# Optimization experiments

Hardware: AMD Instinct MI355X
Metric: run time of the kernel (lower is better)

## Reference

```python
import jax, jax.numpy as jnp
import numpy as np

B, C = 20000, 8          # trees, children (leaves) per tree
WORD, TAG, MEM = 300, 50, 150


def gru_cell(x, h, w_ih, w_hh, b_ih, b_hh):
    # torch.nn.GRUCell math; gate order r, z, n
    gi = x @ w_ih.T + b_ih
    gh = h @ w_hh.T + b_hh
    ir, iz, i_n = jnp.split(gi, 3, axis=-1)
    hr, hz, hn = jnp.split(gh, 3, axis=-1)
    r = jax.nn.sigmoid(ir + hr)
    z = jax.nn.sigmoid(iz + hz)
    n = jnp.tanh(i_n + r * hn)
    return (1.0 - z) * n + z * h


def setup_inputs() -> dict:
    key = jax.random.key(0)
    ks = jax.random.split(key, 16)
    s = 0.05  # small init scale for weights
    return {
        "embs": jax.random.normal(ks[0], (B, C, WORD), jnp.float32),
        "tags": jax.random.normal(ks[1], (B, C, TAG), jnp.float32),
        "tag_parent": jax.random.normal(ks[2], (B, TAG), jnp.float32),
        "w_ih_leaf": jax.random.normal(ks[3], (3 * MEM, WORD + TAG), jnp.float32) * s,
        "w_hh_leaf": jax.random.normal(ks[4], (3 * MEM, MEM), jnp.float32) * s,
        "b_ih_leaf": jax.random.normal(ks[5], (3 * MEM,), jnp.float32) * s,
        "b_hh_leaf": jax.random.normal(ks[6], (3 * MEM,), jnp.float32) * s,
        "w_ih_child": jax.random.normal(ks[7], (3 * MEM, MEM + 2 * TAG), jnp.float32) * s,
        "w_hh_child": jax.random.normal(ks[8], (3 * MEM, MEM), jnp.float32) * s,
        "b_ih_child": jax.random.normal(ks[9], (3 * MEM,), jnp.float32) * s,
        "b_hh_child": jax.random.normal(ks[10], (3 * MEM,), jnp.float32) * s,
        "w_ih_node": jax.random.normal(ks[11], (3 * MEM, 1), jnp.float32) * s,
        "w_hh_node": jax.random.normal(ks[12], (3 * MEM, MEM), jnp.float32) * s,
        "b_ih_node": jax.random.normal(ks[13], (3 * MEM,), jnp.float32) * s,
        "b_hh_node": jax.random.normal(ks[14], (3 * MEM,), jnp.float32) * s,
    }


def reference(embs, tags, tag_parent,
              w_ih_leaf, w_hh_leaf, b_ih_leaf, b_hh_leaf,
              w_ih_child, w_hh_child, b_ih_child, b_hh_child,
              w_ih_node, w_hh_node, b_ih_node, b_hh_node):
    # 1) all leaves at once: GRUCell(concat(word, tag), h=0)  -> [B, C, MEM]
    x_leaf = jnp.concatenate([embs, tags], axis=-1)            # [B, C, WORD+TAG]
    h0 = jnp.zeros((B, C, MEM), x_leaf.dtype)
    leaf_h = gru_cell(x_leaf, h0, w_ih_leaf, w_hh_leaf, b_ih_leaf, b_hh_leaf)

    # 2) child inputs: concat(child state, child tag, parent tag)  -> [B, C, MEM+2*TAG]
    tp = jnp.broadcast_to(tag_parent[:, None, :], (B, C, TAG))
    x_child = jnp.concatenate([leaf_h, tags, tp], axis=-1)

    # 3) sequential left-to-right fold over children with children GRUCell
    def step(h, x_i):
        h_new = gru_cell(x_i, h, w_ih_child, w_hh_child, b_ih_child, b_hh_child)
        return h_new, None

    h_init = jnp.zeros((B, MEM), x_leaf.dtype)
    h_final, _ = jax.lax.scan(step, h_init, jnp.swapaxes(x_child, 0, 1))  # scan over C

    # 4) node GRUCell with x = zeros(1)
    x_zeros = jnp.zeros((B, 1), x_leaf.dtype)
    root = gru_cell(x_zeros, h_final, w_ih_node, w_hh_node, b_ih_node, b_hh_node)
    return root  # [B, MEM]
```

## Files before the change

### kernel.cpp

```cpp
#include <hip/hip_runtime.h>


typedef _Float16 f16;
typedef _Float16 f16x4 __attribute__((ext_vector_type(4)));
typedef _Float16 f16x8 __attribute__((ext_vector_type(8)));
typedef float f32x4 __attribute__((ext_vector_type(4)));

namespace {

constexpr int NTREE = 20000;
constexpr int CCH   = 8;
constexpr int WORD  = 300;
constexpr int TAGD  = 50;
constexpr int MEMD  = 150;
constexpr int NBLK  = 250;
constexpr int LBLK  = 625;

constexpr int KT_L = 11;
constexpr int KT_I = 8;
constexpr int KT_H = 5;
constexpr int KT_N = 5;
constexpr int NTILE = 30;

constexpr size_t OFF_WL   = 0;
constexpr size_t OFF_WI   = OFF_WL + (size_t)KT_L * NTILE * 64 * 16;
constexpr size_t OFF_WH   = OFF_WI + (size_t)KT_I * NTILE * 64 * 16;
constexpr size_t OFF_WN   = OFF_WH + (size_t)KT_H * NTILE * 64 * 16;
constexpr size_t OFF_BIAS = OFF_WN + (size_t)KT_N * NTILE * 64 * 16;
constexpr size_t OFF_DATA = OFF_BIAS + 16 * 160 * 4;

constexpr size_t TG_BYTES = 15360;
constexpr size_t C_STRIDE = (size_t)1250 * TG_BYTES;
constexpr size_t GI_BYTES = (size_t)CCH * C_STRIDE;
constexpr size_t WS_R3    = OFF_DATA + GI_BYTES;
constexpr int    HW_S  = 152;
constexpr size_t WS_R2 = OFF_DATA + (size_t)CCH * NTREE * HW_S * 2;


__device__ __forceinline__ float sigmoid_f(float x) {
  return 1.0f / (1.0f + __expf(-x));
}
__device__ __forceinline__ float tanh_f(float x) {
  float ax = fabsf(x);
  float e  = __expf(-2.0f * ax);
  float t  = (1.0f - e) / (1.0f + e);
  return copysignf(t, x);
}

__global__ void prep_kernel(const float* __restrict__ w_ih_leaf,
                            const float* __restrict__ b_ih_leaf,
                            const float* __restrict__ b_hh_leaf,
                            const float* __restrict__ w_ih_child,
                            const float* __restrict__ w_hh_child,
                            const float* __restrict__ b_ih_child,
                            const float* __restrict__ b_hh_child,
                            const float* __restrict__ w_hh_node,
                            const float* __restrict__ b_ih_node,
                            const float* __restrict__ b_hh_node,
                            char* __restrict__ ws) {
  const int NWL = KT_L * NTILE * 64;
  const int NWI = KT_I * NTILE * 64;
  const int NWH = KT_H * NTILE * 64;
  const int NWN = KT_N * NTILE * 64;
  int t = blockIdx.x * blockDim.x + threadIdx.x;

  if (t < NWL) {
    int kt = t / (NTILE * 64), rem = t % (NTILE * 64);
    int nt = rem / 64, l = rem % 64;
    int gate = nt / 10, jt = nt % 10;
    int j = jt * 16 + (l & 15);
    bool valid = j < MEMD;
    int g = gate * MEMD + (valid ? j : 0);
    f16x8 v;
#pragma unroll
    for (int e = 0; e < 8; ++e) {
      int k = kt * 32 + ((l >> 4) * 8) + e;
      v[e] = (f16)((valid && k < WORD + TAGD) ? w_ih_leaf[g * (WORD + TAGD) + k] : 0.0f);
    }
    ((f16x8*)(ws + OFF_WL))[t] = v;
    return;
  }
  t -= NWL;
  if (t < NWI) {
    int kt = t / (NTILE * 64), rem = t % (NTILE * 64);
    int nt = rem / 64, l = rem % 64;
    int gate = nt / 10, jt = nt % 10;
    int j = jt * 16 + (l & 15);
    bool valid = j < MEMD;
    int g = gate * MEMD + (valid ? j : 0);
    f16x8 v;
#pragma unroll
    for (int e = 0; e < 8; ++e) {
      int k = kt * 32 + ((l >> 4) * 8) + e;
      int src = (k < 150) ? k : (k >= 152 && k < 252) ? (k - 2) : -1;
      v[e] = (f16)((valid && src >= 0) ? w_ih_child[g * 250 + src] : 0.0f);
    }
    ((f16x8*)(ws + OFF_WI))[t] = v;
    return;
  }
  t -= NWI;
  if (t < NWH) {
    int kt = t / (NTILE * 64), rem = t % (NTILE * 64);
    int nt = rem / 64, l = rem % 64;
    int gate = nt / 10, jt = nt % 10;
    int j = jt * 16 + (l & 15);
    bool valid = j < MEMD;
    int g = gate * MEMD + (valid ? j : 0);
    f16x8 v;
#pragma unroll
    for (int e = 0; e < 8; ++e) {
      int k = kt * 32 + ((l >> 4) * 8) + e;
      v[e] = (f16)((valid && k < MEMD) ? w_hh_child[g * MEMD + k] : 0.0f);
    }
    ((f16x8*)(ws + OFF_WH))[t] = v;
    return;
  }
  t -= NWH;
  if (t < NWN) {
    int kt = t / (NTILE * 64), rem = t % (NTILE * 64);
    int nt = rem / 64, l = rem % 64;
    int gate = nt / 10, jt = nt % 10;
    int j = jt * 16 + (l & 15);
    bool valid = j < MEMD;
    int g = gate * MEMD + (valid ? j : 0);
    f16x8 v;
#pragma unroll
    for (int e = 0; e < 8; ++e) {
      int k = kt * 32 + ((l >> 4) * 8) + e;
      v[e] = (f16)((valid && k < MEMD) ? w_hh_node[g * MEMD + k] : 0.0f);
    }
    ((f16x8*)(ws + OFF_WN))[t] = v;
    return;
  }
  t -= NWN;
  if (t < 16 * 160) {
    int arr = t / 160, j = t % 160;
    float v = 0.0f;
    if (j < MEMD) {
      switch (arr) {
        case 0:  v = b_ih_leaf[j] + b_hh_leaf[j]; break;
        case 1:  v = b_ih_leaf[MEMD + j] + b_hh_leaf[MEMD + j]; break;
        case 2:  v = b_ih_leaf[2 * MEMD + j]; break;
        case 3:  v = b_hh_leaf[2 * MEMD + j]; break;
        case 4:  v = b_ih_child[j] + b_hh_child[j]; break;
        case 5:  v = b_ih_child[MEMD + j] + b_hh_child[MEMD + j]; break;
        case 6:  v = b_ih_child[2 * MEMD + j]; break;
        case 7:  v = b_hh_child[2 * MEMD + j]; break;
        case 8:  v = b_ih_node[j] + b_hh_node[j]; break;
        case 9:  v = b_ih_node[MEMD + j] + b_hh_node[MEMD + j]; break;
        case 10: v = b_ih_node[2 * MEMD + j]; break;
        case 11: v = b_hh_node[2 * MEMD + j]; break;
        case 12: v = b_ih_child[j]; break;
        case 13: v = b_ih_child[MEMD + j]; break;
        case 14: v = b_hh_child[j]; break;
        case 15: v = b_hh_child[MEMD + j]; break;
      }
    }
    ((float*)(ws + OFF_BIAS))[arr * 160 + j] = v;
  }
}

__global__ __launch_bounds__(640)
void leaf5_kernel(const float* __restrict__ embs,
                  const float* __restrict__ tags,
                  const float* __restrict__ tag_parent,
                  char* __restrict__ ws) {
  __shared__ f16 xle[32 * 360];
  __shared__ f16 xch[32 * 264];

  const f16x8* WL   = (const f16x8*)(ws + OFF_WL);
  const f16x8* WI   = (const f16x8*)(ws + OFF_WI);
  const float* BIAS = (const float*)(ws + OFF_BIAS);

  const int tid = threadIdx.x, lane = tid & 63, w = tid >> 6;
  const int blk = blockIdx.x, c = blockIdx.y, t0 = blk * 32;
  const int arow = lane & 15, acol8 = (lane >> 4) * 8, qrow = (lane >> 4) * 4;
  const int j = w * 16 + arow;
  const bool jok = j < MEMD;

  for (int i = tid; i < 32 * 75; i += 640) {
    int r = i / 75, k4 = i - r * 75;
    float4 v = *(const float4*)(embs + ((size_t)(t0 + r) * CCH + c) * WORD + 4 * k4);
    f16* p = xle + r * 360 + 4 * k4;
    p[0] = (f16)v.x; p[1] = (f16)v.y; p[2] = (f16)v.z; p[3] = (f16)v.w;
  }
  for (int i = tid; i < 32 * 25; i += 640) {
    int r = i / 25, k2 = i - r * 25;
    float2 v = *(const float2*)(tags + ((size_t)(t0 + r) * CCH + c) * TAGD + 2 * k2);
    xle[r * 360 + 300 + 2 * k2]     = (f16)v.x;
    xle[r * 360 + 300 + 2 * k2 + 1] = (f16)v.y;
  }
  for (int i = tid; i < 32 * 25; i += 640) {
    int r = i / 25, k2 = i - r * 25;
    float2 v = *(const float2*)(tag_parent + (size_t)(t0 + r) * TAGD + 2 * k2);
    xch[r * 264 + 202 + 2 * k2] = (f16)v.x;
    xch[r * 264 + 203 + 2 * k2] = (f16)v.y;
  }
  for (int i = tid; i < 32 * 6; i += 640) {
    int r = i / 6, k = i - r * 6;
    int col = (k < 2) ? (150 + k) : (250 + k);
    xch[r * 264 + col] = (f16)0.0f;
  }
  if (tid < 32) {
    xle[tid * 360 + 350] = (f16)0.0f;
    xle[tid * 360 + 351] = (f16)0.0f;
  }
  __syncthreads();

  for (int i = tid; i < 32 * 50; i += 640) {
    int r = i / 50, tt = i - r * 50;
    xch[r * 264 + 152 + tt] = xle[r * 360 + 300 + tt];
  }

  f32x4 acc[3][2];
#pragma unroll
  for (int g = 0; g < 3; ++g) { acc[g][0] = 0.f; acc[g][1] = 0.f; }

  for (int kt = 0; kt < KT_L; ++kt) {
    f16x8 a0 = *(const f16x8*)(xle + kt * 32 + acol8 + (arow)      * 360);
    f16x8 a1 = *(const f16x8*)(xle + kt * 32 + acol8 + (16 + arow) * 360);
#pragma unroll
    for (int g = 0; g < 3; ++g) {
      f16x8 b = WL[(kt * NTILE + g * 10 + w) * 64 + lane];
      acc[g][0] = __builtin_amdgcn_mfma_f32_16x16x32_f16(a0, b, acc[g][0], 0, 0, 0);
      acc[g][1] = __builtin_amdgcn_mfma_f32_16x16x32_f16(a1, b, acc[g][1], 0, 0, 0);
    }
  }

  {
    const float bLr = BIAS[j], bLz = BIAS[160 + j];
    const float bLi = BIAS[320 + j], bLh = BIAS[480 + j];
#pragma unroll
    for (int m = 0; m < 2; ++m)
#pragma unroll
      for (int q = 0; q < 4; ++q) {
        int row = 16 * m + qrow + q;
        float rg = sigmoid_f(acc[0][m][q] + bLr);
        float zg = sigmoid_f(acc[1][m][q] + bLz);
        float ng = tanh_f(acc[2][m][q] + bLi + rg * bLh);
        if (jok) xch[row * 264 + j] = (f16)((1.0f - zg) * ng);
      }
  }
  __syncthreads();

#pragma unroll
  for (int g = 0; g < 3; ++g) { acc[g][0] = 0.f; acc[g][1] = 0.f; }

  for (int kt = 0; kt < KT_I; ++kt) {
    f16x8 a0 = *(const f16x8*)(xch + kt * 32 + acol8 + (arow)      * 264);
    f16x8 a1 = *(const f16x8*)(xch + kt * 32 + acol8 + (16 + arow) * 264);
#pragma unroll
    for (int g = 0; g < 3; ++g) {
      f16x8 b = WI[(kt * NTILE + g * 10 + w) * 64 + lane];
      acc[g][0] = __builtin_amdgcn_mfma_f32_16x16x32_f16(a0, b, acc[g][0], 0, 0, 0);
      acc[g][1] = __builtin_amdgcn_mfma_f32_16x16x32_f16(a1, b, acc[g][1], 0, 0, 0);
    }
  }

  {
    const float bi[3] = {BIAS[12 * 160 + j], BIAS[13 * 160 + j], BIAS[6 * 160 + j]};
#pragma unroll
    for (int m = 0; m < 2; ++m) {
      int tg = blk * 2 + m;
      char* base = ws + OFF_DATA + (size_t)c * C_STRIDE + (size_t)tg * TG_BYTES +
                   (size_t)lane * 8;
#pragma unroll
      for (int g = 0; g < 3; ++g) {
        f16x4 v;
#pragma unroll
        for (int q = 0; q < 4; ++q) v[q] = (f16)(acc[g][m][q] + bi[g]);
        *(f16x4*)(base + (size_t)(g * 10 + w) * 512) = v;
      }
    }
  }
}

__global__ __launch_bounds__(640, 3)
void fold3_kernel(const char* __restrict__ ws,
                  float* __restrict__ out) {
  __shared__ f16 hls[80 * 168];

  const f16x8* WH   = (const f16x8*)(ws + OFF_WH);
  const f16x8* WN   = (const f16x8*)(ws + OFF_WN);
  const float* BIAS = (const float*)(ws + OFF_BIAS);

  const int tid = threadIdx.x, lane = tid & 63, w = tid >> 6;
  const int blk = blockIdx.x, t0 = blk * 80;
  const int arow = lane & 15, acol8 = (lane >> 4) * 8, qrow = (lane >> 4) * 4;
  const int j = w * 16 + arow;
  const bool jok = j < MEMD;

  const float bhr = BIAS[14 * 160 + j], bhz = BIAS[15 * 160 + j], bhn = BIAS[7 * 160 + j];
  const float bNr = BIAS[8 * 160 + j],  bNz = BIAS[9 * 160 + j];
  const float bNi = BIAS[10 * 160 + j], bNh = BIAS[11 * 160 + j];

  for (int i = tid; i < 80 * 18; i += 640) {
    int r = i / 18;
    hls[r * 168 + 150 + (i - r * 18)] = (f16)0.0f;
  }

  f16x8 whr[5];
#pragma unroll
  for (int kt = 0; kt < KT_H; ++kt) whr[kt] = WH[(kt * NTILE + w) * 64 + lane];

  const char* gbase = ws + OFF_DATA + (size_t)(blk * 5) * TG_BYTES +
                      (size_t)w * 512 + (size_t)lane * 8;

  f32x4 hp[5];
#pragma unroll
  for (int m = 0; m < 5; ++m) hp[m] = 0.f;

#pragma unroll
  for (int c = 0; c < CCH; ++c) {
    f16x4 gbuf[15];
#pragma unroll
    for (int m = 0; m < 5; ++m)
#pragma unroll
      for (int g = 0; g < 3; ++g)
        gbuf[m * 3 + g] = *(const f16x4*)(gbase + (size_t)c * C_STRIDE +
                                          (size_t)m * TG_BYTES + (size_t)g * 5120);

    f32x4 aR[5], aZ[5], aNh[5];
#pragma unroll
    for (int m = 0; m < 5; ++m) { aR[m] = 0.f; aZ[m] = 0.f; aNh[m] = 0.f; }

    if (c != 0) {
      for (int kt = 0; kt < KT_H; ++kt) {
        f16x8 bz = WH[(kt * NTILE + 10 + w) * 64 + lane];
        f16x8 bn = WH[(kt * NTILE + 20 + w) * 64 + lane];
        const f16* ab = hls + kt * 32 + acol8;
#pragma unroll
        for (int m = 0; m < 5; ++m) {
          f16x8 a = *(const f16x8*)(ab + (16 * m + arow) * 168);
          aR[m]  = __builtin_amdgcn_mfma_f32_16x16x32_f16(a, whr[kt], aR[m], 0, 0, 0);
          aZ[m]  = __builtin_amdgcn_mfma_f32_16x16x32_f16(a, bz, aZ[m], 0, 0, 0);
          aNh[m] = __builtin_amdgcn_mfma_f32_16x16x32_f16(a, bn, aNh[m], 0, 0, 0);
        }
      }
      __syncthreads();
    }

#pragma unroll
    for (int m = 0; m < 5; ++m)
#pragma unroll
      for (int q = 0; q < 4; ++q) {
        int row = 16 * m + qrow + q;
        float rg = sigmoid_f((float)gbuf[m * 3 + 0][q] + aR[m][q] + bhr);
        float zg = sigmoid_f((float)gbuf[m * 3 + 1][q] + aZ[m][q] + bhz);
        float ng = tanh_f((float)gbuf[m * 3 + 2][q] + rg * (aNh[m][q] + bhn));
        float h  = (1.0f - zg) * ng + zg * hp[m][q];
        hp[m][q] = h;
        if (jok) hls[row * 168 + j] = (f16)h;
      }
    __syncthreads();
  }

  f32x4 aR[5], aZ[5], aNh[5];
#pragma unroll
  for (int m = 0; m < 5; ++m) { aR[m] = 0.f; aZ[m] = 0.f; aNh[m] = 0.f; }
  for (int kt = 0; kt < KT_N; ++kt) {
    f16x8 br = WN[(kt * NTILE + w) * 64 + lane];
    f16x8 bz = WN[(kt * NTILE + 10 + w) * 64 + lane];
    f16x8 bn = WN[(kt * NTILE + 20 + w) * 64 + lane];
    const f16* ab = hls + kt * 32 + acol8;
#pragma unroll
    for (int m = 0; m < 5; ++m) {
      f16x8 a = *(const f16x8*)(ab + (16 * m + arow) * 168);
      aR[m]  = __builtin_amdgcn_mfma_f32_16x16x32_f16(a, br, aR[m], 0, 0, 0);
      aZ[m]  = __builtin_amdgcn_mfma_f32_16x16x32_f16(a, bz, aZ[m], 0, 0, 0);
      aNh[m] = __builtin_amdgcn_mfma_f32_16x16x32_f16(a, bn, aNh[m], 0, 0, 0);
    }
  }
#pragma unroll
  for (int m = 0; m < 5; ++m)
#pragma unroll
    for (int q = 0; q < 4; ++q) {
      int row = 16 * m + qrow + q;
      float rg = sigmoid_f(aR[m][q] + bNr);
      float zg = sigmoid_f(aZ[m][q] + bNz);
      float ng = tanh_f(bNi + rg * (aNh[m][q] + bNh));
      float o  = (1.0f - zg) * ng + zg * hp[m][q];
      if (jok) out[(size_t)(t0 + row) * MEMD + j] = o;
    }
}

namespace r2 {

__global__ __launch_bounds__(640)
void leaf_kernel(const float* __restrict__ embs,
                 const float* __restrict__ tags,
                 char* __restrict__ ws) {
  __shared__ f16 xle[80 * 360];
  const f16x8* WL   = (const f16x8*)(ws + OFF_WL);
  const float* BIAS = (const float*)(ws + OFF_BIAS);
  f16* hws = (f16*)(ws + OFF_DATA);

  const int tid = threadIdx.x, lane = tid & 63, w = tid >> 6;
  const int c = blockIdx.y, t0 = blockIdx.x * 80;
  const int arow = lane & 15, acol8 = (lane >> 4) * 8, qrow = (lane >> 4) * 4;
  const int j = w * 16 + (lane & 15);

  for (int i = tid; i < 80 * 150; i += 640) {
    int r = i / 150, k2 = i - r * 150;
    float2 v = *(const float2*)(embs + ((size_t)(t0 + r) * CCH + c) * WORD + 2 * k2);
    xle[r * 360 + 2 * k2]     = (f16)v.x;
    xle[r * 360 + 2 * k2 + 1] = (f16)v.y;
  }
  for (int i = tid; i < 80 * 25; i += 640) {
    int r = i / 25, k2 = i - r * 25;
    float2 v = *(const float2*)(tags + ((size_t)(t0 + r) * CCH + c) * TAGD + 2 * k2);
    xle[r * 360 + 300 + 2 * k2]     = (f16)v.x;
    xle[r * 360 + 300 + 2 * k2 + 1] = (f16)v.y;
  }
  for (int i = tid; i < 80; i += 640) {
    xle[i * 360 + 350] = (f16)0.0f;
    xle[i * 360 + 351] = (f16)0.0f;
  }
  __syncthreads();

  f32x4 aR[5], aZ[5], aN[5];
#pragma unroll
  for (int m = 0; m < 5; ++m) { aR[m] = 0.f; aZ[m] = 0.f; aN[m] = 0.f; }
  for (int kt = 0; kt < KT_L; ++kt) {
    f16x8 br = WL[(kt * NTILE + w) * 64 + lane];
    f16x8 bz = WL[(kt * NTILE + 10 + w) * 64 + lane];
    f16x8 bn = WL[(kt * NTILE + 20 + w) * 64 + lane];
    const f16* ab = xle + kt * 32 + acol8;
#pragma unroll
    for (int m = 0; m < 5; ++m) {
      f16x8 a = *(const f16x8*)(ab + (16 * m + arow) * 360);
      aR[m] = __builtin_amdgcn_mfma_f32_16x16x32_f16(a, br, aR[m], 0, 0, 0);
      aZ[m] = __builtin_amdgcn_mfma_f32_16x16x32_f16(a, bz, aZ[m], 0, 0, 0);
      aN[m] = __builtin_amdgcn_mfma_f32_16x16x32_f16(a, bn, aN[m], 0, 0, 0);
    }
  }
  const float bLr = BIAS[j], bLz = BIAS[160 + j], bLi = BIAS[320 + j], bLh = BIAS[480 + j];
#pragma unroll
  for (int m = 0; m < 5; ++m) {
#pragma unroll
    for (int q = 0; q < 4; ++q) {
      int row = 16 * m + qrow + q;
      float rg = sigmoid_f(aR[m][q] + bLr);
      float zg = sigmoid_f(aZ[m][q] + bLz);
      float ng = tanh_f(aN[m][q] + bLi + rg * bLh);
      float h  = (1.0f - zg) * ng;
      if (j < HW_S)
        hws[((size_t)c * NTREE + t0 + row) * HW_S + j] = (f16)(j < MEMD ? h : 0.0f);
    }
  }
}

__global__ __launch_bounds__(640)
void fold_kernel(const float* __restrict__ tags,
                 const float* __restrict__ tag_parent,
                 const char* __restrict__ ws,
                 float* __restrict__ out) {
  extern __shared__ char fsm[];
  f16* xch0 = (f16*)fsm;
  f16* xch1 = xch0 + 80 * 264;
  f16* hls  = xch1 + 80 * 264;

  const f16x8* WI   = (const f16x8*)(ws + OFF_WI);
  const f16x8* WH   = (const f16x8*)(ws + OFF_WH);
  const f16x8* WN   = (const f16x8*)(ws + OFF_WN);
  const float* BIAS = (const float*)(ws + OFF_BIAS);
  const f16*   hws  = (const f16*)(ws + OFF_DATA);

  const int tid = threadIdx.x, lane = tid & 63, w = tid >> 6;
  const int t0 = blockIdx.x * 80;
  const int arow = lane & 15, acol8 = (lane >> 4) * 8, qrow = (lane >> 4) * 4;
  const int j = w * 16 + (lane & 15);
  const bool jok = j < MEMD;

  const float bCr = BIAS[4 * 160 + j], bCz = BIAS[5 * 160 + j];
  const float bCi = BIAS[6 * 160 + j], bCh = BIAS[7 * 160 + j];
  const float bNr = BIAS[8 * 160 + j], bNz = BIAS[9 * 160 + j];
  const float bNi = BIAS[10 * 160 + j], bNh = BIAS[11 * 160 + j];

  for (int i = tid; i < 1680; i += 640) ((int4*)hls)[i] = make_int4(0, 0, 0, 0);
  for (int i = tid; i < 80 * 25; i += 640) {
    int r = i / 25, k2 = i - r * 25;
    float2 v = *(const float2*)(tag_parent + (size_t)(t0 + r) * TAGD + 2 * k2);
    f16 a = (f16)v.x, b = (f16)v.y;
    xch0[r * 264 + 202 + 2 * k2] = a; xch0[r * 264 + 203 + 2 * k2] = b;
    xch1[r * 264 + 202 + 2 * k2] = a; xch1[r * 264 + 203 + 2 * k2] = b;
  }
  for (int i = tid; i < 80 * 4; i += 640) {
    int r = i >> 2, k = i & 3;
    xch0[r * 264 + 252 + k] = (f16)0.0f;
    xch1[r * 264 + 252 + k] = (f16)0.0f;
  }
#pragma unroll
  for (int s = 0; s < 3; ++s) {
    int i = tid + 640 * s;
    if (i < 1520) {
      int r = i / 19, q = i - r * 19;
      *(f16x8*)(xch0 + r * 264 + 8 * q) =
          *(const f16x8*)(hws + ((size_t)(t0 + r)) * HW_S + 8 * q);
    }
  }
#pragma unroll
  for (int s = 0; s < 4; ++s) {
    int i = tid + 640 * s;
    if (i < 2000) {
      int r = i / 25, k2 = i - r * 25;
      float2 v = *(const float2*)(tags + ((size_t)(t0 + r) * CCH) * TAGD + 2 * k2);
      xch0[r * 264 + 152 + 2 * k2] = (f16)v.x;
      xch0[r * 264 + 153 + 2 * k2] = (f16)v.y;
    }
  }
  __syncthreads();

  f32x4 hp[5];
#pragma unroll
  for (int m = 0; m < 5; ++m) hp[m] = 0.f;

  f16* xc = xch0;
  f16* xa = xch1;

  for (int c = 0; c < CCH; ++c) {
    f16x8 ph[3];
    float2 pt[4];
    if (c < 7) {
#pragma unroll
      for (int s = 0; s < 3; ++s) {
        int i = tid + 640 * s;
        if (i < 1520) {
          int r = i / 19, q = i - r * 19;
          ph[s] = *(const f16x8*)(hws + ((size_t)(c + 1) * NTREE + t0 + r) * HW_S + 8 * q);
        }
      }
#pragma unroll
      for (int s = 0; s < 4; ++s) {
        int i = tid + 640 * s;
        if (i < 2000) {
          int r = i / 25, k2 = i - r * 25;
          pt[s] = *(const float2*)(tags + ((size_t)(t0 + r) * CCH + (c + 1)) * TAGD + 2 * k2);
        }
      }
    }

    f32x4 aR[5], aZ[5], aNi[5], aNh[5];
#pragma unroll
    for (int m = 0; m < 5; ++m) { aR[m] = 0.f; aZ[m] = 0.f; aNi[m] = 0.f; aNh[m] = 0.f; }
    for (int kt = 0; kt < KT_I; ++kt) {
      f16x8 br = WI[(kt * NTILE + w) * 64 + lane];
      f16x8 bz = WI[(kt * NTILE + 10 + w) * 64 + lane];
      f16x8 bn = WI[(kt * NTILE + 20 + w) * 64 + lane];
      const f16* ab = xc + kt * 32 + acol8;
#pragma unroll
      for (int m = 0; m < 5; ++m) {
        f16x8 a = *(const f16x8*)(ab + (16 * m + arow) * 264);
        aR[m]  = __builtin_amdgcn_mfma_f32_16x16x32_f16(a, br, aR[m], 0, 0, 0);
        aZ[m]  = __builtin_amdgcn_mfma_f32_16x16x32_f16(a, bz, aZ[m], 0, 0, 0);
        aNi[m] = __builtin_amdgcn_mfma_f32_16x16x32_f16(a, bn, aNi[m], 0, 0, 0);
      }
    }
    for (int kt = 0; kt < KT_H; ++kt) {
      f16x8 br = WH[(kt * NTILE + w) * 64 + lane];
      f16x8 bz = WH[(kt * NTILE + 10 + w) * 64 + lane];
      f16x8 bn = WH[(kt * NTILE + 20 + w) * 64 + lane];
      const f16* ab = hls + kt * 32 + acol8;
#pragma unroll
      for (int m = 0; m < 5; ++m) {
        f16x8 a = *(const f16x8*)(ab + (16 * m + arow) * 168);
        aR[m]  = __builtin_amdgcn_mfma_f32_16x16x32_f16(a, br, aR[m], 0, 0, 0);
        aZ[m]  = __builtin_amdgcn_mfma_f32_16x16x32_f16(a, bz, aZ[m], 0, 0, 0);
        aNh[m] = __builtin_amdgcn_mfma_f32_16x16x32_f16(a, bn, aNh[m], 0, 0, 0);
      }
    }
    __syncthreads();

    if (c < 7) {
#pragma unroll
      for (int s = 0; s < 3; ++s) {
        int i = tid + 640 * s;
        if (i < 1520) {
          int r = i / 19, q = i - r * 19;
          *(f16x8*)(xa + r * 264 + 8 * q) = ph[s];
        }
      }
#pragma unroll
      for (int s = 0; s < 4; ++s) {
        int i = tid + 640 * s;
        if (i < 2000) {
          int r = i / 25, k2 = i - r * 25;
          xa[r * 264 + 152 + 2 * k2] = (f16)pt[s].x;
          xa[r * 264 + 153 + 2 * k2] = (f16)pt[s].y;
        }
      }
    }

#pragma unroll
    for (int m = 0; m < 5; ++m) {
#pragma unroll
      for (int q = 0; q < 4; ++q) {
        int row = 16 * m + qrow + q;
        float rg = sigmoid_f(aR[m][q] + bCr);
        float zg = sigmoid_f(aZ[m][q] + bCz);
        float ng = tanh_f(aNi[m][q] + bCi + rg * (aNh[m][q] + bCh));
        float h  = (1.0f - zg) * ng + zg * hp[m][q];
        hp[m][q] = h;
        if (jok) hls[row * 168 + j] = (f16)h;
      }
    }
    __syncthreads();
    f16* tsw = xc; xc = xa; xa = tsw;
  }

  f32x4 aR[5], aZ[5], aNh[5];
#pragma unroll
  for (int m = 0; m < 5; ++m) { aR[m] = 0.f; aZ[m] = 0.f; aNh[m] = 0.f; }
  for (int kt = 0; kt < KT_N; ++kt) {
    f16x8 br = WN[(kt * NTILE + w) * 64 + lane];
    f16x8 bz = WN[(kt * NTILE + 10 + w) * 64 + lane];
    f16x8 bn = WN[(kt * NTILE + 20 + w) * 64 + lane];
    const f16* ab = hls + kt * 32 + acol8;
#pragma unroll
    for (int m = 0; m < 5; ++m) {
      f16x8 a = *(const f16x8*)(ab + (16 * m + arow) * 168);
      aR[m]  = __builtin_amdgcn_mfma_f32_16x16x32_f16(a, br, aR[m], 0, 0, 0);
      aZ[m]  = __builtin_amdgcn_mfma_f32_16x16x32_f16(a, bz, aZ[m], 0, 0, 0);
      aNh[m] = __builtin_amdgcn_mfma_f32_16x16x32_f16(a, bn, aNh[m], 0, 0, 0);
    }
  }
#pragma unroll
  for (int m = 0; m < 5; ++m) {
#pragma unroll
    for (int q = 0; q < 4; ++q) {
      int row = 16 * m + qrow + q;
      float rg = sigmoid_f(aR[m][q] + bNr);
      float zg = sigmoid_f(aZ[m][q] + bNz);
      float ng = tanh_f(bNi + rg * (aNh[m][q] + bNh));
      float o  = (1.0f - zg) * ng + zg * hp[m][q];
      if (jok) out[(size_t)(t0 + row) * MEMD + j] = o;
    }
  }
}

}

}

extern "C" void kernel_launch(void* const* d_in, const int* in_sizes, int n_in,
                              void* d_out, int out_size, void* d_ws, size_t ws_size,
                              hipStream_t stream) {
  const float* embs       = (const float*)d_in[0];
  const float* tags       = (const float*)d_in[1];
  const float* tag_parent = (const float*)d_in[2];
  const float* w_ih_leaf  = (const float*)d_in[3];
  const float* b_ih_leaf  = (const float*)d_in[5];
  const float* b_hh_leaf  = (const float*)d_in[6];
  const float* w_ih_child = (const float*)d_in[7];
  const float* w_hh_child = (const float*)d_in[8];
  const float* b_ih_child = (const float*)d_in[9];
  const float* b_hh_child = (const float*)d_in[10];
  const float* w_hh_node  = (const float*)d_in[12];
  const float* b_ih_node  = (const float*)d_in[13];
  const float* b_hh_node  = (const float*)d_in[14];
  float* out = (float*)d_out;
  char*  ws  = (char*)d_ws;

  prep_kernel<<<228, 256, 0, stream>>>(w_ih_leaf, b_ih_leaf, b_hh_leaf,
                                       w_ih_child, w_hh_child, b_ih_child, b_hh_child,
                                       w_hh_node, b_ih_node, b_hh_node, ws);

  if (ws_size >= WS_R3) {
    leaf5_kernel<<<dim3(LBLK, CCH), 640, 0, stream>>>(embs, tags, tag_parent, ws);
    fold3_kernel<<<NBLK, 640, 0, stream>>>(ws, out);
  } else {
    r2::leaf_kernel<<<dim3(NBLK, CCH), 640, 0, stream>>>(embs, tags, ws);
    constexpr int FOLD_LDS = (2 * 80 * 264 + 80 * 168) * 2;
    hipFuncSetAttribute((const void*)r2::fold_kernel,
                        hipFuncAttributeMaxDynamicSharedMemorySize, FOLD_LDS);
    r2::fold_kernel<<<NBLK, 640, FOLD_LDS, stream>>>(tags, tag_parent, ws, out);
  }
}
```

Measured before the change: 425.9 us.

## Double leaf tile to 64 rows with shared LDS buffer; keep fold weights in registers

The leaf kernel now handles 64 trees per block instead of 32, so each weight B-fragment loaded from global memory feeds four MFMAs instead of two. The leaf and child input tiles share one LDS buffer, with tag and parent-tag reloads done after the leaf GEMM. A partial last block is handled by clamping input rows and guarding the stores. The fold kernel preloads all three hidden-weight gate fragments into registers and drops its occupancy hint to 1, trading register pressure for fewer global loads inside the sequential loop.

```diff
diff --git a/kernel.cpp b/kernel.cpp
--- a/kernel.cpp
+++ b/kernel.cpp
@@ -14,7 +14,7 @@
 constexpr int TAGD  = 50;
 constexpr int MEMD  = 150;
 constexpr int NBLK  = 250;
-constexpr int LBLK  = 625;
+constexpr int LBLK  = 313;
 
 constexpr int KT_L = 11;
 constexpr int KT_I = 8;
@@ -161,77 +161,71 @@
 }
 
 __global__ __launch_bounds__(640)
-void leaf5_kernel(const float* __restrict__ embs,
+void leaf6_kernel(const float* __restrict__ embs,
                   const float* __restrict__ tags,
                   const float* __restrict__ tag_parent,
                   char* __restrict__ ws) {
-  __shared__ f16 xle[32 * 360];
-  __shared__ f16 xch[32 * 264];
+  __shared__ f16 buf[64 * 360];
+  f16* xle = buf;
+  f16* xch = buf;
 
   const f16x8* WL   = (const f16x8*)(ws + OFF_WL);
   const f16x8* WI   = (const f16x8*)(ws + OFF_WI);
   const float* BIAS = (const float*)(ws + OFF_BIAS);
 
   const int tid = threadIdx.x, lane = tid & 63, w = tid >> 6;
-  const int blk = blockIdx.x, c = blockIdx.y, t0 = blk * 32;
+  const int blk = blockIdx.x, c = blockIdx.y, t0 = blk * 64;
   const int arow = lane & 15, acol8 = (lane >> 4) * 8, qrow = (lane >> 4) * 4;
   const int j = w * 16 + arow;
   const bool jok = j < MEMD;
 
-  for (int i = tid; i < 32 * 75; i += 640) {
+  for (int i = tid; i < 64 * 75; i += 640) {
     int r = i / 75, k4 = i - r * 75;
-    float4 v = *(const float4*)(embs + ((size_t)(t0 + r) * CCH + c) * WORD + 4 * k4);
+    int row = min(t0 + r, NTREE - 1);
+    float4 v = *(const float4*)(embs + ((size_t)row * CCH + c) * WORD + 4 * k4);
     f16* p = xle + r * 360 + 4 * k4;
     p[0] = (f16)v.x; p[1] = (f16)v.y; p[2] = (f16)v.z; p[3] = (f16)v.w;
   }
-  for (int i = tid; i < 32 * 25; i += 640) {
+  for (int i = tid; i < 64 * 25; i += 640) {
     int r = i / 25, k2 = i - r * 25;
-    float2 v = *(const float2*)(tags + ((size_t)(t0 + r) * CCH + c) * TAGD + 2 * k2);
+    int row = min(t0 + r, NTREE - 1);
+    float2 v = *(const float2*)(tags + ((size_t)row * CCH + c) * TAGD + 2 * k2);
     xle[r * 360 + 300 + 2 * k2]     = (f16)v.x;
     xle[r * 360 + 300 + 2 * k2 + 1] = (f16)v.y;
   }
-  for (int i = tid; i < 32 * 25; i += 640) {
-    int r = i / 25, k2 = i - r * 25;
-    float2 v = *(const float2*)(tag_parent + (size_t)(t0 + r) * TAGD + 2 * k2);
-    xch[r * 264 + 202 + 2 * k2] = (f16)v.x;
-    xch[r * 264 + 203 + 2 * k2] = (f16)v.y;
-  }
-  for (int i = tid; i < 32 * 6; i += 640) {
-    int r = i / 6, k = i - r * 6;
-    int col = (k < 2) ? (150 + k) : (250 + k);
-    xch[r * 264 + col] = (f16)0.0f;
-  }
-  if (tid < 32) {
+  if (tid < 64) {
     xle[tid * 360 + 350] = (f16)0.0f;
     xle[tid * 360 + 351] = (f16)0.0f;
   }
   __syncthreads();
 
-  for (int i = tid; i < 32 * 50; i += 640) {
-    int r = i / 50, tt = i - r * 50;
-    xch[r * 264 + 152 + tt] = xle[r * 360 + 300 + tt];
-  }
-
-  f32x4 acc[3][2];
-#pragma unroll
-  for (int g = 0; g < 3; ++g) { acc[g][0] = 0.f; acc[g][1] = 0.f; }
+  f32x4 acc[3][4];
+#pragma unroll
+  for (int g = 0; g < 3; ++g)
+#pragma unroll
+    for (int m = 0; m < 4; ++m) acc[g][m] = 0.f;
 
   for (int kt = 0; kt < KT_L; ++kt) {
     f16x8 a0 = *(const f16x8*)(xle + kt * 32 + acol8 + (arow)      * 360);
     f16x8 a1 = *(const f16x8*)(xle + kt * 32 + acol8 + (16 + arow) * 360);
+    f16x8 a2 = *(const f16x8*)(xle + kt * 32 + acol8 + (32 + arow) * 360);
+    f16x8 a3 = *(const f16x8*)(xle + kt * 32 + acol8 + (48 + arow) * 360);
 #pragma unroll
     for (int g = 0; g < 3; ++g) {
       f16x8 b = WL[(kt * NTILE + g * 10 + w) * 64 + lane];
       acc[g][0] = __builtin_amdgcn_mfma_f32_16x16x32_f16(a0, b, acc[g][0], 0, 0, 0);
       acc[g][1] = __builtin_amdgcn_mfma_f32_16x16x32_f16(a1, b, acc[g][1], 0, 0, 0);
-    }
-  }
+      acc[g][2] = __builtin_amdgcn_mfma_f32_16x16x32_f16(a2, b, acc[g][2], 0, 0, 0);
+      acc[g][3] = __builtin_amdgcn_mfma_f32_16x16x32_f16(a3, b, acc[g][3], 0, 0, 0);
+    }
+  }
+  __syncthreads();
 
   {
     const float bLr = BIAS[j], bLz = BIAS[160 + j];
     const float bLi = BIAS[320 + j], bLh = BIAS[480 + j];
 #pragma unroll
-    for (int m = 0; m < 2; ++m)
+    for (int m = 0; m < 4; ++m)
 #pragma unroll
       for (int q = 0; q < 4; ++q) {
         int row = 16 * m + qrow + q;
@@ -241,42 +235,69 @@
         if (jok) xch[row * 264 + j] = (f16)((1.0f - zg) * ng);
       }
   }
+  for (int i = tid; i < 64 * 25; i += 640) {
+    int r = i / 25, k2 = i - r * 25;
+    int row = min(t0 + r, NTREE - 1);
+    float2 v = *(const float2*)(tags + ((size_t)row * CCH + c) * TAGD + 2 * k2);
+    xch[r * 264 + 152 + 2 * k2] = (f16)v.x;
+    xch[r * 264 + 153 + 2 * k2] = (f16)v.y;
+  }
+  for (int i = tid; i < 64 * 25; i += 640) {
+    int r = i / 25, k2 = i - r * 25;
+    int row = min(t0 + r, NTREE - 1);
+    float2 v = *(const float2*)(tag_parent + (size_t)row * TAGD + 2 * k2);
+    xch[r * 264 + 202 + 2 * k2] = (f16)v.x;
+    xch[r * 264 + 203 + 2 * k2] = (f16)v.y;
+  }
+  for (int i = tid; i < 64 * 6; i += 640) {
+    int r = i / 6, k = i - r * 6;
+    int col = (k < 2) ? (150 + k) : (250 + k);
+    xch[r * 264 + col] = (f16)0.0f;
+  }
   __syncthreads();
 
 #pragma unroll
-  for (int g = 0; g < 3; ++g) { acc[g][0] = 0.f; acc[g][1] = 0.f; }
+  for (int g = 0; g < 3; ++g)
+#pragma unroll
+    for (int m = 0; m < 4; ++m) acc[g][m] = 0.f;
 
   for (int kt = 0; kt < KT_I; ++kt) {
     f16x8 a0 = *(const f16x8*)(xch + kt * 32 + acol8 + (arow)      * 264);
     f16x8 a1 = *(const f16x8*)(xch + kt * 32 + acol8 + (16 + arow) * 264);
+    f16x8 a2 = *(const f16x8*)(xch + kt * 32 + acol8 + (32 + arow) * 264);
+    f16x8 a3 = *(const f16x8*)(xch + kt * 32 + acol8 + (48 + arow) * 264);
 #pragma unroll
     for (int g = 0; g < 3; ++g) {
       f16x8 b = WI[(kt * NTILE + g * 10 + w) * 64 + lane];
       acc[g][0] = __builtin_amdgcn_mfma_f32_16x16x32_f16(a0, b, acc[g][0], 0, 0, 0);
       acc[g][1] = __builtin_amdgcn_mfma_f32_16x16x32_f16(a1, b, acc[g][1], 0, 0, 0);
+      acc[g][2] = __builtin_amdgcn_mfma_f32_16x16x32_f16(a2, b, acc[g][2], 0, 0, 0);
+      acc[g][3] = __builtin_amdgcn_mfma_f32_16x16x32_f16(a3, b, acc[g][3], 0, 0, 0);
     }
   }
 
   {
     const float bi[3] = {BIAS[12 * 160 + j], BIAS[13 * 160 + j], BIAS[6 * 160 + j]};
 #pragma unroll
-    for (int m = 0; m < 2; ++m) {
-      int tg = blk * 2 + m;
-      char* base = ws + OFF_DATA + (size_t)c * C_STRIDE + (size_t)tg * TG_BYTES +
-                   (size_t)lane * 8;
-#pragma unroll
-      for (int g = 0; g < 3; ++g) {
-        f16x4 v;
-#pragma unroll
-        for (int q = 0; q < 4; ++q) v[q] = (f16)(acc[g][m][q] + bi[g]);
-        *(f16x4*)(base + (size_t)(g * 10 + w) * 512) = v;
-      }
-    }
-  }
-}
-
-__global__ __launch_bounds__(640, 3)
-void fold3_kernel(const char* __restrict__ ws,
+    for (int m = 0; m < 4; ++m) {
+      if (t0 + 16 * m < NTREE) {
+        int tg = blk * 4 + m;
+        char* base = ws + OFF_DATA + (size_t)c * C_STRIDE + (size_t)tg * TG_BYTES +
+                     (size_t)lane * 8;
+#pragma unroll
+        for (int g = 0; g < 3; ++g) {
+          f16x4 v;
+#pragma unroll
+          for (int q = 0; q < 4; ++q) v[q] = (f16)(acc[g][m][q] + bi[g]);
+          *(f16x4*)(base + (size_t)(g * 10 + w) * 512) = v;
+        }
+      }
+    }
+  }
+}
+
+__global__ __launch_bounds__(640, 1)
+void fold6_kernel(const char* __restrict__ ws,
                   float* __restrict__ out) {
   __shared__ f16 hls[80 * 168];
 
@@ -299,9 +320,13 @@
     hls[r * 168 + 150 + (i - r * 18)] = (f16)0.0f;
   }
 
-  f16x8 whr[5];
-#pragma unroll
-  for (int kt = 0; kt < KT_H; ++kt) whr[kt] = WH[(kt * NTILE + w) * 64 + lane];
+  f16x8 whr[5], whz[5], whn[5];
+#pragma unroll
+  for (int kt = 0; kt < KT_H; ++kt) {
+    whr[kt] = WH[(kt * NTILE + w) * 64 + lane];
+    whz[kt] = WH[(kt * NTILE + 10 + w) * 64 + lane];
+    whn[kt] = WH[(kt * NTILE + 20 + w) * 64 + lane];
+  }
 
   const char* gbase = ws + OFF_DATA + (size_t)(blk * 5) * TG_BYTES +
                       (size_t)w * 512 + (size_t)lane * 8;
@@ -325,16 +350,15 @@
     for (int m = 0; m < 5; ++m) { aR[m] = 0.f; aZ[m] = 0.f; aNh[m] = 0.f; }
 
     if (c != 0) {
+#pragma unroll
       for (int kt = 0; kt < KT_H; ++kt) {
-        f16x8 bz = WH[(kt * NTILE + 10 + w) * 64 + lane];
-        f16x8 bn = WH[(kt * NTILE + 20 + w) * 64 + lane];
         const f16* ab = hls + kt * 32 + acol8;
 #pragma unroll
         for (int m = 0; m < 5; ++m) {
           f16x8 a = *(const f16x8*)(ab + (16 * m + arow) * 168);
           aR[m]  = __builtin_amdgcn_mfma_f32_16x16x32_f16(a, whr[kt], aR[m], 0, 0, 0);
-          aZ[m]  = __builtin_amdgcn_mfma_f32_16x16x32_f16(a, bz, aZ[m], 0, 0, 0);
-          aNh[m] = __builtin_amdgcn_mfma_f32_16x16x32_f16(a, bn, aNh[m], 0, 0, 0);
+          aZ[m]  = __builtin_amdgcn_mfma_f32_16x16x32_f16(a, whz[kt], aZ[m], 0, 0, 0);
+          aNh[m] = __builtin_amdgcn_mfma_f32_16x16x32_f16(a, whn[kt], aNh[m], 0, 0, 0);
         }
       }
       __syncthreads();
@@ -666,13 +690,13 @@
                                        w_hh_node, b_ih_node, b_hh_node, ws);
 
   if (ws_size >= WS_R3) {
-    leaf5_kernel<<<dim3(LBLK, CCH), 640, 0, stream>>>(embs, tags, tag_parent, ws);
-    fold3_kernel<<<NBLK, 640, 0, stream>>>(ws, out);
+    leaf6_kernel<<<dim3(LBLK, CCH), 640, 0, stream>>>(embs, tags, tag_parent, ws);
+    fold6_kernel<<<NBLK, 640, 0, stream>>>(ws, out);
   } else {
-    r2::leaf_kernel<<<dim3(NBLK, CCH), 640, 0, stream>>>(embs, tags, ws);
+    r2::leaf_kernel<<<dim3(250, CCH), 640, 0, stream>>>(embs, tags, ws);
     constexpr int FOLD_LDS = (2 * 80 * 264 + 80 * 168) * 2;
     hipFuncSetAttribute((const void*)r2::fold_kernel,
                         hipFuncAttributeMaxDynamicSharedMemorySize, FOLD_LDS);
-    r2::fold_kernel<<<NBLK, 640, FOLD_LDS, stream>>>(tags, tag_parent, ws, out);
-  }
-}
+    r2::fold_kernel<<<250, 640, FOLD_LDS, stream>>>(tags, tag_parent, ws, out);
+  }
+}
```

New measurement: 391.1 us. -8.2%, faster.

## Loop leaf kernel over children with register prefetch; preload all fold weights

Applied to the files above, without the earlier changes.

The leaf kernel now has each block process all 8 children in a loop instead of one child per grid-y slice. It prefetches the next child's embeddings and tags into registers while computing the current one, and reuses a single shared buffer for both stages. The fold kernel keeps all three recurrent weight slices in registers instead of reloading z/n weights every step, and its launch bounds drop to one block per SM. This trades grid parallelism (625 blocks instead of 5000) and higher register pressure for latency hiding and fewer redundant loads.

```diff
diff --git a/kernel.cpp b/kernel.cpp
--- a/kernel.cpp
+++ b/kernel.cpp
@@ -161,75 +161,96 @@
 }
 
 __global__ __launch_bounds__(640)
-void leaf5_kernel(const float* __restrict__ embs,
+void leaf7_kernel(const float* __restrict__ embs,
                   const float* __restrict__ tags,
                   const float* __restrict__ tag_parent,
                   char* __restrict__ ws) {
-  __shared__ f16 xle[32 * 360];
-  __shared__ f16 xch[32 * 264];
+  __shared__ f16 buf[32 * 360];
+  f16* xle = buf;
+  f16* xch = buf;
 
   const f16x8* WL   = (const f16x8*)(ws + OFF_WL);
   const f16x8* WI   = (const f16x8*)(ws + OFF_WI);
   const float* BIAS = (const float*)(ws + OFF_BIAS);
 
   const int tid = threadIdx.x, lane = tid & 63, w = tid >> 6;
-  const int blk = blockIdx.x, c = blockIdx.y, t0 = blk * 32;
+  const int blk = blockIdx.x, t0 = blk * 32;
   const int arow = lane & 15, acol8 = (lane >> 4) * 8, qrow = (lane >> 4) * 4;
   const int j = w * 16 + arow;
   const bool jok = j < MEMD;
 
-  for (int i = tid; i < 32 * 75; i += 640) {
-    int r = i / 75, k4 = i - r * 75;
-    float4 v = *(const float4*)(embs + ((size_t)(t0 + r) * CCH + c) * WORD + 4 * k4);
-    f16* p = xle + r * 360 + 4 * k4;
-    p[0] = (f16)v.x; p[1] = (f16)v.y; p[2] = (f16)v.z; p[3] = (f16)v.w;
-  }
-  for (int i = tid; i < 32 * 25; i += 640) {
-    int r = i / 25, k2 = i - r * 25;
-    float2 v = *(const float2*)(tags + ((size_t)(t0 + r) * CCH + c) * TAGD + 2 * k2);
-    xle[r * 360 + 300 + 2 * k2]     = (f16)v.x;
-    xle[r * 360 + 300 + 2 * k2 + 1] = (f16)v.y;
-  }
-  for (int i = tid; i < 32 * 25; i += 640) {
-    int r = i / 25, k2 = i - r * 25;
-    float2 v = *(const float2*)(tag_parent + (size_t)(t0 + r) * TAGD + 2 * k2);
-    xch[r * 264 + 202 + 2 * k2] = (f16)v.x;
-    xch[r * 264 + 203 + 2 * k2] = (f16)v.y;
-  }
-  for (int i = tid; i < 32 * 6; i += 640) {
-    int r = i / 6, k = i - r * 6;
-    int col = (k < 2) ? (150 + k) : (250 + k);
-    xch[r * 264 + col] = (f16)0.0f;
-  }
-  if (tid < 32) {
-    xle[tid * 360 + 350] = (f16)0.0f;
-    xle[tid * 360 + 351] = (f16)0.0f;
-  }
-  __syncthreads();
-
-  for (int i = tid; i < 32 * 50; i += 640) {
-    int r = i / 50, tt = i - r * 50;
-    xch[r * 264 + 152 + tt] = xle[r * 360 + 300 + tt];
-  }
-
-  f32x4 acc[3][2];
-#pragma unroll
-  for (int g = 0; g < 3; ++g) { acc[g][0] = 0.f; acc[g][1] = 0.f; }
-
-  for (int kt = 0; kt < KT_L; ++kt) {
-    f16x8 a0 = *(const f16x8*)(xle + kt * 32 + acol8 + (arow)      * 360);
-    f16x8 a1 = *(const f16x8*)(xle + kt * 32 + acol8 + (16 + arow) * 360);
-#pragma unroll
-    for (int g = 0; g < 3; ++g) {
-      f16x8 b = WL[(kt * NTILE + g * 10 + w) * 64 + lane];
-      acc[g][0] = __builtin_amdgcn_mfma_f32_16x16x32_f16(a0, b, acc[g][0], 0, 0, 0);
-      acc[g][1] = __builtin_amdgcn_mfma_f32_16x16x32_f16(a1, b, acc[g][1], 0, 0, 0);
-    }
-  }
-
-  {
-    const float bLr = BIAS[j], bLz = BIAS[160 + j];
-    const float bLi = BIAS[320 + j], bLh = BIAS[480 + j];
+  const float bLr = BIAS[j], bLz = BIAS[160 + j];
+  const float bLi = BIAS[320 + j], bLh = BIAS[480 + j];
+  const float biC[3] = {BIAS[12 * 160 + j], BIAS[13 * 160 + j], BIAS[6 * 160 + j]};
+
+  const int ie0 = tid, ie1 = tid + 640, ie2 = tid + 1280, ie3 = tid + 1920;
+  const int it0 = tid, it1 = tid + 640;
+
+  float2 tp0 = make_float2(0, 0), tp1 = make_float2(0, 0);
+  if (it0 < 800) {
+    int r = it0 / 25, k2 = it0 - (it0 / 25) * 25;
+    tp0 = *(const float2*)(tag_parent + (size_t)(t0 + r) * TAGD + 2 * k2);
+  }
+  if (it1 < 800) {
+    int r = it1 / 25, k2 = it1 - (it1 / 25) * 25;
+    tp1 = *(const float2*)(tag_parent + (size_t)(t0 + r) * TAGD + 2 * k2);
+  }
+
+  float4 pe0, pe1, pe2, pe3;
+  float2 pt0, pt1;
+#define LOADC(cc)                                                                        \
+  {                                                                                      \
+    if (ie0 < 2400) { int r = ie0 / 75, k = ie0 - r * 75;                                \
+      pe0 = *(const float4*)(embs + ((size_t)(t0 + r) * CCH + (cc)) * WORD + 4 * k); }   \
+    if (ie1 < 2400) { int r = ie1 / 75, k = ie1 - r * 75;                                \
+      pe1 = *(const float4*)(embs + ((size_t)(t0 + r) * CCH + (cc)) * WORD + 4 * k); }   \
+    if (ie2 < 2400) { int r = ie2 / 75, k = ie2 - r * 75;                                \
+      pe2 = *(const float4*)(embs + ((size_t)(t0 + r) * CCH + (cc)) * WORD + 4 * k); }   \
+    if (ie3 < 2400) { int r = ie3 / 75, k = ie3 - r * 75;                                \
+      pe3 = *(const float4*)(embs + ((size_t)(t0 + r) * CCH + (cc)) * WORD + 4 * k); }   \
+    if (it0 < 800)  { int r = it0 / 25, k2 = it0 - r * 25;                               \
+      pt0 = *(const float2*)(tags + ((size_t)(t0 + r) * CCH + (cc)) * TAGD + 2 * k2); }  \
+    if (it1 < 800)  { int r = it1 / 25, k2 = it1 - r * 25;                               \
+      pt1 = *(const float2*)(tags + ((size_t)(t0 + r) * CCH + (cc)) * TAGD + 2 * k2); }  \
+  }
+
+  LOADC(0);
+
+#pragma unroll
+  for (int c = 0; c < CCH; ++c) {
+    if (ie0 < 2400) { int r = ie0 / 75, k = ie0 - (ie0 / 75) * 75; f16* p = xle + r * 360 + 4 * k;
+      p[0] = (f16)pe0.x; p[1] = (f16)pe0.y; p[2] = (f16)pe0.z; p[3] = (f16)pe0.w; }
+    if (ie1 < 2400) { int r = ie1 / 75, k = ie1 - (ie1 / 75) * 75; f16* p = xle + r * 360 + 4 * k;
+      p[0] = (f16)pe1.x; p[1] = (f16)pe1.y; p[2] = (f16)pe1.z; p[3] = (f16)pe1.w; }
+    if (ie2 < 2400) { int r = ie2 / 75, k = ie2 - (ie2 / 75) * 75; f16* p = xle + r * 360 + 4 * k;
+      p[0] = (f16)pe2.x; p[1] = (f16)pe2.y; p[2] = (f16)pe2.z; p[3] = (f16)pe2.w; }
+    if (ie3 < 2400) { int r = ie3 / 75, k = ie3 - (ie3 / 75) * 75; f16* p = xle + r * 360 + 4 * k;
+      p[0] = (f16)pe3.x; p[1] = (f16)pe3.y; p[2] = (f16)pe3.z; p[3] = (f16)pe3.w; }
+    if (it0 < 800) { int r = it0 / 25, k2 = it0 - (it0 / 25) * 25;
+      xle[r * 360 + 300 + 2 * k2] = (f16)pt0.x; xle[r * 360 + 301 + 2 * k2] = (f16)pt0.y; }
+    if (it1 < 800) { int r = it1 / 25, k2 = it1 - (it1 / 25) * 25;
+      xle[r * 360 + 300 + 2 * k2] = (f16)pt1.x; xle[r * 360 + 301 + 2 * k2] = (f16)pt1.y; }
+    if (tid < 32) { xle[tid * 360 + 350] = (f16)0.0f; xle[tid * 360 + 351] = (f16)0.0f; }
+    float2 ct0 = pt0, ct1 = pt1;
+    __syncthreads();
+
+    if (c < CCH - 1) LOADC(c + 1);
+
+    f32x4 acc[3][2];
+#pragma unroll
+    for (int g = 0; g < 3; ++g) { acc[g][0] = 0.f; acc[g][1] = 0.f; }
+    for (int kt = 0; kt < KT_L; ++kt) {
+      f16x8 a0 = *(const f16x8*)(xle + kt * 32 + acol8 + (arow)      * 360);
+      f16x8 a1 = *(const f16x8*)(xle + kt * 32 + acol8 + (16 + arow) * 360);
+#pragma unroll
+      for (int g = 0; g < 3; ++g) {
+        f16x8 b = WL[(kt * NTILE + g * 10 + w) * 64 + lane];
+        acc[g][0] = __builtin_amdgcn_mfma_f32_16x16x32_f16(a0, b, acc[g][0], 0, 0, 0);
+        acc[g][1] = __builtin_amdgcn_mfma_f32_16x16x32_f16(a1, b, acc[g][1], 0, 0, 0);
+      }
+    }
+    __syncthreads();
+
 #pragma unroll
     for (int m = 0; m < 2; ++m)
 #pragma unroll
@@ -240,25 +261,32 @@
         float ng = tanh_f(acc[2][m][q] + bLi + rg * bLh);
         if (jok) xch[row * 264 + j] = (f16)((1.0f - zg) * ng);
       }
-  }
-  __syncthreads();
-
-#pragma unroll
-  for (int g = 0; g < 3; ++g) { acc[g][0] = 0.f; acc[g][1] = 0.f; }
-
-  for (int kt = 0; kt < KT_I; ++kt) {
-    f16x8 a0 = *(const f16x8*)(xch + kt * 32 + acol8 + (arow)      * 264);
-    f16x8 a1 = *(const f16x8*)(xch + kt * 32 + acol8 + (16 + arow) * 264);
-#pragma unroll
-    for (int g = 0; g < 3; ++g) {
-      f16x8 b = WI[(kt * NTILE + g * 10 + w) * 64 + lane];
-      acc[g][0] = __builtin_amdgcn_mfma_f32_16x16x32_f16(a0, b, acc[g][0], 0, 0, 0);
-      acc[g][1] = __builtin_amdgcn_mfma_f32_16x16x32_f16(a1, b, acc[g][1], 0, 0, 0);
-    }
-  }
-
-  {
-    const float bi[3] = {BIAS[12 * 160 + j], BIAS[13 * 160 + j], BIAS[6 * 160 + j]};
+    if (it0 < 800) { int r = it0 / 25, k2 = it0 - (it0 / 25) * 25;
+      xch[r * 264 + 152 + 2 * k2] = (f16)ct0.x; xch[r * 264 + 153 + 2 * k2] = (f16)ct0.y;
+      xch[r * 264 + 202 + 2 * k2] = (f16)tp0.x; xch[r * 264 + 203 + 2 * k2] = (f16)tp0.y; }
+    if (it1 < 800) { int r = it1 / 25, k2 = it1 - (it1 / 25) * 25;
+      xch[r * 264 + 152 + 2 * k2] = (f16)ct1.x; xch[r * 264 + 153 + 2 * k2] = (f16)ct1.y;
+      xch[r * 264 + 202 + 2 * k2] = (f16)tp1.x; xch[r * 264 + 203 + 2 * k2] = (f16)tp1.y; }
+    for (int i = tid; i < 32 * 6; i += 640) {
+      int r = i / 6, k = i - r * 6;
+      int col = (k < 2) ? (150 + k) : (250 + k);
+      xch[r * 264 + col] = (f16)0.0f;
+    }
+    __syncthreads();
+
+#pragma unroll
+    for (int g = 0; g < 3; ++g) { acc[g][0] = 0.f; acc[g][1] = 0.f; }
+    for (int kt = 0; kt < KT_I; ++kt) {
+      f16x8 a0 = *(const f16x8*)(xch + kt * 32 + acol8 + (arow)      * 264);
+      f16x8 a1 = *(const f16x8*)(xch + kt * 32 + acol8 + (16 + arow) * 264);
+#pragma unroll
+      for (int g = 0; g < 3; ++g) {
+        f16x8 b = WI[(kt * NTILE + g * 10 + w) * 64 + lane];
+        acc[g][0] = __builtin_amdgcn_mfma_f32_16x16x32_f16(a0, b, acc[g][0], 0, 0, 0);
+        acc[g][1] = __builtin_amdgcn_mfma_f32_16x16x32_f16(a1, b, acc[g][1], 0, 0, 0);
+      }
+    }
+
 #pragma unroll
     for (int m = 0; m < 2; ++m) {
       int tg = blk * 2 + m;
@@ -268,15 +296,17 @@
       for (int g = 0; g < 3; ++g) {
         f16x4 v;
 #pragma unroll
-        for (int q = 0; q < 4; ++q) v[q] = (f16)(acc[g][m][q] + bi[g]);
+        for (int q = 0; q < 4; ++q) v[q] = (f16)(acc[g][m][q] + biC[g]);
         *(f16x4*)(base + (size_t)(g * 10 + w) * 512) = v;
       }
     }
-  }
-}
-
-__global__ __launch_bounds__(640, 3)
-void fold3_kernel(const char* __restrict__ ws,
+    __syncthreads();
+  }
+#undef LOADC
+}
+
+__global__ __launch_bounds__(640, 1)
+void fold6_kernel(const char* __restrict__ ws,
                   float* __restrict__ out) {
   __shared__ f16 hls[80 * 168];
 
@@ -299,9 +329,13 @@
     hls[r * 168 + 150 + (i - r * 18)] = (f16)0.0f;
   }
 
-  f16x8 whr[5];
-#pragma unroll
-  for (int kt = 0; kt < KT_H; ++kt) whr[kt] = WH[(kt * NTILE + w) * 64 + lane];
+  f16x8 whr[5], whz[5], whn[5];
+#pragma unroll
+  for (int kt = 0; kt < KT_H; ++kt) {
+    whr[kt] = WH[(kt * NTILE + w) * 64 + lane];
+    whz[kt] = WH[(kt * NTILE + 10 + w) * 64 + lane];
+    whn[kt] = WH[(kt * NTILE + 20 + w) * 64 + lane];
+  }
 
   const char* gbase = ws + OFF_DATA + (size_t)(blk * 5) * TG_BYTES +
                       (size_t)w * 512 + (size_t)lane * 8;
@@ -325,16 +359,15 @@
     for (int m = 0; m < 5; ++m) { aR[m] = 0.f; aZ[m] = 0.f; aNh[m] = 0.f; }
 
     if (c != 0) {
+#pragma unroll
       for (int kt = 0; kt < KT_H; ++kt) {
-        f16x8 bz = WH[(kt * NTILE + 10 + w) * 64 + lane];
-        f16x8 bn = WH[(kt * NTILE + 20 + w) * 64 + lane];
         const f16* ab = hls + kt * 32 + acol8;
 #pragma unroll
         for (int m = 0; m < 5; ++m) {
           f16x8 a = *(const f16x8*)(ab + (16 * m + arow) * 168);
           aR[m]  = __builtin_amdgcn_mfma_f32_16x16x32_f16(a, whr[kt], aR[m], 0, 0, 0);
-          aZ[m]  = __builtin_amdgcn_mfma_f32_16x16x32_f16(a, bz, aZ[m], 0, 0, 0);
-          aNh[m] = __builtin_amdgcn_mfma_f32_16x16x32_f16(a, bn, aNh[m], 0, 0, 0);
+          aZ[m]  = __builtin_amdgcn_mfma_f32_16x16x32_f16(a, whz[kt], aZ[m], 0, 0, 0);
+          aNh[m] = __builtin_amdgcn_mfma_f32_16x16x32_f16(a, whn[kt], aNh[m], 0, 0, 0);
         }
       }
       __syncthreads();
@@ -666,13 +699,13 @@
                                        w_hh_node, b_ih_node, b_hh_node, ws);
 
   if (ws_size >= WS_R3) {
-    leaf5_kernel<<<dim3(LBLK, CCH), 640, 0, stream>>>(embs, tags, tag_parent, ws);
-    fold3_kernel<<<NBLK, 640, 0, stream>>>(ws, out);
+    leaf7_kernel<<<LBLK, 640, 0, stream>>>(embs, tags, tag_parent, ws);
+    fold6_kernel<<<NBLK, 640, 0, stream>>>(ws, out);
   } else {
-    r2::leaf_kernel<<<dim3(NBLK, CCH), 640, 0, stream>>>(embs, tags, ws);
+    r2::leaf_kernel<<<dim3(250, CCH), 640, 0, stream>>>(embs, tags, ws);
     constexpr int FOLD_LDS = (2 * 80 * 264 + 80 * 168) * 2;
     hipFuncSetAttribute((const void*)r2::fold_kernel,
                         hipFuncAttributeMaxDynamicSharedMemorySize, FOLD_LDS);
-    r2::fold_kernel<<<NBLK, 640, FOLD_LDS, stream>>>(tags, tag_parent, ws, out);
-  }
-}
+    r2::fold_kernel<<<250, 640, FOLD_LDS, stream>>>(tags, tag_parent, ws, out);
+  }
+}
```

New measurement: 738.8 us. 1.73x slower.
